# Performance work log

Measured on AMD Instinct MI355X. Metric: run time of the kernel, lower is better.

Reference implementation:

```python
import jax, jax.numpy as jnp
import numpy as np

HIDDEN = 3072
N_HEADS = 24
N_KV = 8
HEAD_DIM = HIDDEN // N_HEADS          # 128
ROT = int(HEAD_DIM * 0.75)            # 96 (partial rotary)
OP_SIZE = N_HEADS * HEAD_DIM + 2 * N_KV * HEAD_DIM  # 5120
LORA_R = 256
LORA_SCALE = 512.0 / LORA_R           # 2.0
ROPE_THETA = 10000.0
SCALE = HEAD_DIM ** -0.5


def setup_inputs() -> dict:
    key = jax.random.key(0)
    ks = jax.random.split(key, 8)
    B, S = 2, 2048
    hidden_states = jax.random.normal(ks[0], (B, S, HIDDEN), dtype=jnp.float32)
    position_ids = jnp.arange(B * S, dtype=jnp.int64 if jax.config.jax_enable_x64 else jnp.int32).reshape(B, S)
    w = lambda k, o, i: jax.random.normal(k, (o, i), dtype=jnp.float32) * (i ** -0.5)
    return {
        "hidden_states": hidden_states,
        "Wqkv": w(ks[1], OP_SIZE, HIDDEN),
        "Aqkv": w(ks[2], LORA_R, HIDDEN),
        "Bqkv": w(ks[3], OP_SIZE, LORA_R) * 0.01,
        "Wo": w(ks[4], HIDDEN, N_HEADS * HEAD_DIM),
        "Ao": w(ks[5], LORA_R, N_HEADS * HEAD_DIM),
        "Bo": w(ks[6], HIDDEN, LORA_R) * 0.01,
        "position_ids": position_ids,
    }


def _lora_linear(x, W, A, Bm):
    # base GEMM + low-rank LoRA update, scaling = alpha/r
    return x @ W.T + (x @ A.T) @ Bm.T * LORA_SCALE


def _rotate_half(x):
    h = x.shape[-1] // 2
    return jnp.concatenate((-x[..., h:], x[..., :h]), axis=-1)


def reference(hidden_states, Wqkv, Aqkv, Bqkv, Wo, Ao, Bo, position_ids):
    B, S, _ = hidden_states.shape
    qkv = _lora_linear(hidden_states, Wqkv, Aqkv, Bqkv)  # [B,S,5120]
    q_pos = N_HEADS * HEAD_DIM
    kv_pos = N_KV * HEAD_DIM
    q = qkv[..., :q_pos].reshape(B, S, N_HEADS, HEAD_DIM)
    k = qkv[..., q_pos:q_pos + kv_pos].reshape(B, S, N_KV, HEAD_DIM)
    v = qkv[..., q_pos + kv_pos:].reshape(B, S, N_KV, HEAD_DIM)

    # partial RoPE: cos/sin cache over rotary_ndims=96
    inv_freq = 1.0 / (ROPE_THETA ** (jnp.arange(0, ROT, 2, dtype=jnp.float32) / ROT))  # [48]
    freqs = position_ids.astype(jnp.float32)[..., None] * inv_freq  # [B,S,48]
    emb = jnp.concatenate((freqs, freqs), axis=-1)                   # [B,S,96]
    cos = jnp.cos(emb)[:, :, None, :]  # broadcast over head axis (bsnd)
    sin = jnp.sin(emb)[:, :, None, :]

    def rope(x):
        xr, xp = x[..., :ROT], x[..., ROT:]
        xr = xr * cos + _rotate_half(xr) * sin
        return jnp.concatenate((xr, xp), axis=-1)

    q = rope(q)
    k = rope(k)

    # GQA: repeat kv heads to match query heads
    groups = N_HEADS // N_KV
    k = jnp.repeat(k, groups, axis=2)
    v = jnp.repeat(v, groups, axis=2)

    scores = jnp.einsum('bqhd,bkhd->bhqk', q, k) * SCALE  # [B,H,S,S]
    causal = jnp.tril(jnp.ones((S, S), dtype=bool))
    scores = jnp.where(causal, scores, jnp.finfo(scores.dtype).min)
    probs = jax.nn.softmax(scores, axis=-1)
    attn = jnp.einsum('bhqk,bkhd->bqhd', probs, v).reshape(B, S, N_HEADS * HEAD_DIM)
    return _lora_linear(attn, Wo, Ao, Bo)
```

## Files before the change

kernel.cpp:

```cpp
#include <hip/hip_runtime.h>

typedef unsigned short u16;
typedef unsigned int   u32;

typedef __bf16 bf16_t;
typedef bf16_t bf16x8 __attribute__((ext_vector_type(8)));
typedef float  f32x4  __attribute__((ext_vector_type(4)));
typedef float  f32x16 __attribute__((ext_vector_type(16)));
typedef u16    u16x8  __attribute__((ext_vector_type(8)));
typedef u32    u32x4  __attribute__((ext_vector_type(4)));

__device__ __forceinline__ float bf2f(u16 u) { return __uint_as_float(((u32)u) << 16); }
__device__ __forceinline__ u16 f2bf(float f) {
  u32 u = __float_as_uint(f);
  u32 r = u + 0x7fffu + ((u >> 16) & 1u);
  return (u16)(r >> 16);
}
__device__ __forceinline__ float fast_exp2(float x) { return __builtin_amdgcn_exp2f(x); }

__device__ __forceinline__ void gload_lds16(const u16* g, u16* l) {
  __builtin_amdgcn_global_load_lds(
      (const __attribute__((address_space(1))) void*)g,
      (__attribute__((address_space(3))) void*)l,
      16, 0, 0);
}

#define SBAR0() __builtin_amdgcn_sched_barrier(0)
#define HWBAR() __builtin_amdgcn_s_barrier()

__global__ void k_cast_all(const float* __restrict__ x,  const float* __restrict__ wq,
                           const float* __restrict__ bq, const float* __restrict__ aq,
                           const float* __restrict__ wo, const float* __restrict__ bo,
                           const float* __restrict__ ao,
                           u16* __restrict__ xw, u16* __restrict__ wwq, u16* __restrict__ aqkvb,
                           u16* __restrict__ wwo, u16* __restrict__ aob) {
  const int total = 5177344;
  int i = blockIdx.x * blockDim.x + threadIdx.x;
  const int stride = gridDim.x * blockDim.x;
  for (; i < total; i += stride) {
    const float* src; u16* dst; int C8, L, off, loc;
    if      (i < 1572864) { src = x;  dst = xw;    C8 = 384; L = 3328; off = 0;    loc = i; }
    else if (i < 3538944) { src = wq; dst = wwq;   C8 = 384; L = 3328; off = 0;    loc = i - 1572864; }
    else if (i < 3702784) { src = bq; dst = wwq;   C8 = 32;  L = 3328; off = 3072; loc = i - 3538944; }
    else if (i < 3801088) { src = aq; dst = aqkvb; C8 = 384; L = 3072; off = 0;    loc = i - 3702784; }
    else if (i < 4980736) { src = wo; dst = wwo;   C8 = 384; L = 3328; off = 0;    loc = i - 3801088; }
    else if (i < 5079040) { src = bo; dst = wwo;   C8 = 32;  L = 3328; off = 3072; loc = i - 4980736; }
    else                  { src = ao; dst = aob;   C8 = 384; L = 3072; off = 0;    loc = i - 5079040; }
    const int r = loc / C8, c8 = loc - r * C8;
    const f32x4* p = (const f32x4*)(src + ((size_t)r * C8 + c8) * 8);
    f32x4 a = p[0], b2 = p[1];
    u16x8 o;
    o[0] = f2bf(a[0]);  o[1] = f2bf(a[1]);  o[2] = f2bf(a[2]);  o[3] = f2bf(a[3]);
    o[4] = f2bf(b2[0]); o[5] = f2bf(b2[1]); o[6] = f2bf(b2[2]); o[7] = f2bf(b2[3]);
    *(u16x8*)(dst + (size_t)r * L + off + c8 * 8) = o;
  }
}

__global__ void k_red4_cast(const float* __restrict__ t4, u16* __restrict__ out,
                            int C8, int L, int off, float scale, size_t plane) {
  const int r  = blockIdx.y;
  const int c8 = blockIdx.x * 64 + threadIdx.x;
  if (c8 >= C8) return;
  size_t base = (size_t)r * (C8 * 8) + c8 * 8;
  float s[8];
#pragma unroll
  for (int j = 0; j < 8; ++j) s[j] = 0.f;
#pragma unroll
  for (int p = 0; p < 4; ++p) {
    const f32x4* q = (const f32x4*)(t4 + p * plane + base);
    f32x4 a = q[0], b = q[1];
    s[0] += a[0]; s[1] += a[1]; s[2] += a[2]; s[3] += a[3];
    s[4] += b[0]; s[5] += b[1]; s[6] += b[2]; s[7] += b[3];
  }
  u16x8 o;
#pragma unroll
  for (int j = 0; j < 8; ++j) o[j] = f2bf(s[j] * scale);
  *(u16x8*)(out + (size_t)r * L + off + c8 * 8) = o;
}

__global__ __launch_bounds__(256) void k_gemm_bt_sk(
    const u16* __restrict__ A, const u16* __restrict__ B, float* __restrict__ C,
    int M, int N, int lda, int ldb, int kc) {
  __shared__ u16 As[64][64 + 8];
  __shared__ u16 Bs[64][64 + 8];
  const int tid   = threadIdx.x;
  const int lane  = tid & 63;
  const int w     = tid >> 6;
  const int wm    = (w >> 1) * 32;
  const int wn    = (w & 1) * 32;
  const int row16 = lane & 15;
  const int quad  = lane >> 4;
  const int m0 = blockIdx.y * 64;
  const int n0 = blockIdx.x * 64;
  const int ldr = tid >> 2;
  const int ldc = (tid & 3) * 16;
  const int z   = blockIdx.z;
  float* Cz = C + (size_t)z * M * N;
  const int kbeg = z * kc, kend = kbeg + kc;

  f32x4 acc[2][2] = {};

  for (int k0 = kbeg; k0 < kend; k0 += 64) {
    const u16* ga = A + (size_t)(m0 + ldr) * lda + (k0 + ldc);
    const u16* gb = B + (size_t)(n0 + ldr) * ldb + (k0 + ldc);
    u16x8 a0 = *(const u16x8*)ga;
    u16x8 a1 = *(const u16x8*)(ga + 8);
    u16x8 b0 = *(const u16x8*)gb;
    u16x8 b1 = *(const u16x8*)(gb + 8);
    __syncthreads();
    *(u16x8*)&As[ldr][ldc]     = a0;
    *(u16x8*)&As[ldr][ldc + 8] = a1;
    *(u16x8*)&Bs[ldr][ldc]     = b0;
    *(u16x8*)&Bs[ldr][ldc + 8] = b1;
    __syncthreads();
#pragma unroll
    for (int kk = 0; kk < 64; kk += 32) {
      bf16x8 af0 = *(const bf16x8*)&As[wm + row16][kk + quad * 8];
      bf16x8 af1 = *(const bf16x8*)&As[wm + 16 + row16][kk + quad * 8];
      bf16x8 bg0 = *(const bf16x8*)&Bs[wn + row16][kk + quad * 8];
      bf16x8 bg1 = *(const bf16x8*)&Bs[wn + 16 + row16][kk + quad * 8];
      acc[0][0] = __builtin_amdgcn_mfma_f32_16x16x32_bf16(af0, bg0, acc[0][0], 0, 0, 0);
      acc[0][1] = __builtin_amdgcn_mfma_f32_16x16x32_bf16(af0, bg1, acc[0][1], 0, 0, 0);
      acc[1][0] = __builtin_amdgcn_mfma_f32_16x16x32_bf16(af1, bg0, acc[1][0], 0, 0, 0);
      acc[1][1] = __builtin_amdgcn_mfma_f32_16x16x32_bf16(af1, bg1, acc[1][1], 0, 0, 0);
    }
  }
#pragma unroll
  for (int tm = 0; tm < 2; ++tm)
#pragma unroll
    for (int tn = 0; tn < 2; ++tn) {
      int gm = m0 + wm + tm * 16 + quad * 4;
      int gn = n0 + wn + tn * 16 + row16;
#pragma unroll
      for (int r = 0; r < 4; ++r)
        Cz[(size_t)(gm + r) * N + gn] = acc[tm][tn][r];
    }
}

__device__ __forceinline__ void stage_half(
    int H, int nt4,
    const u16* __restrict__ A, const u16* __restrict__ B, int K,
    int m0, int n0, u16* AsB, u16* BsB,
    int w, int rowin, int colsw) {
  if (H >= nt4) return;
  const int t = H >> 2, slot = H & 3;
  const int half = slot & 1;
  const u16* G = (slot < 2) ? A : B;
  const int r0 = (slot < 2) ? m0 : n0;
  u16* lds = ((slot < 2) ? AsB : BsB) + (t & 1) * 16384 + half * 8192;
  const int k0 = t * 64;
#pragma unroll
  for (int i = 0; i < 2; ++i) {
    const int chunk = w * 2 + i;
    const int row = half * 128 + chunk * 8 + rowin;
    gload_lds16(G + (size_t)(r0 + row) * K + k0 + colsw, lds + chunk * 512);
  }
}

__device__ __forceinline__ bf16x8 frag_ld(const u16* base, int row, int c16) {
  return *(const bf16x8*)(base + row * 64 + ((c16 ^ (row & 7)) << 3));
}

template <int RB>
__device__ __forceinline__ void gemm256_group(
    int k, int nt,
    const u16* __restrict__ A, const u16* __restrict__ B, int K,
    int m0, int n0, u16* AsB, u16* BsB,
    int wr, int wc, int row16, int quad, int w, int rowin, int colsw,
    f32x4 (&acc)[8][4]) {
  const u16* Ab = AsB + RB * 16384;
  const u16* Bb = BsB + RB * 16384;
  const int nt4 = nt * 4;
  bf16x8 a0[4][2], a1[4][2], b0[2][2], b1[2][2];

#pragma unroll
  for (int mf = 0; mf < 4; ++mf)
#pragma unroll
    for (int kk = 0; kk < 2; ++kk)
      a0[mf][kk] = frag_ld(Ab, wr * 128 + mf * 16 + row16, kk * 4 + quad);
#pragma unroll
  for (int nf = 0; nf < 2; ++nf)
#pragma unroll
    for (int kk = 0; kk < 2; ++kk)
      b0[nf][kk] = frag_ld(Bb, wc * 64 + nf * 16 + row16, kk * 4 + quad);
  stage_half(4 * k + 5, nt4, A, B, K, m0, n0, AsB, BsB, w, rowin, colsw);
  SBAR0(); HWBAR(); SBAR0();
  __builtin_amdgcn_s_setprio(1);
#pragma unroll
  for (int mf = 0; mf < 4; ++mf)
#pragma unroll
    for (int nf = 0; nf < 2; ++nf)
#pragma unroll
      for (int kk = 0; kk < 2; ++kk)
        acc[mf][nf] = __builtin_amdgcn_mfma_f32_16x16x32_bf16(a0[mf][kk], b0[nf][kk], acc[mf][nf], 0, 0, 0);
  __builtin_amdgcn_s_setprio(0);
  SBAR0(); HWBAR(); SBAR0();

#pragma unroll
  for (int nf = 0; nf < 2; ++nf)
#pragma unroll
    for (int kk = 0; kk < 2; ++kk)
      b1[nf][kk] = frag_ld(Bb, wc * 64 + 32 + nf * 16 + row16, kk * 4 + quad);
  stage_half(4 * k + 6, nt4, A, B, K, m0, n0, AsB, BsB, w, rowin, colsw);
  SBAR0(); HWBAR(); SBAR0();
  __builtin_amdgcn_s_setprio(1);
#pragma unroll
  for (int mf = 0; mf < 4; ++mf)
#pragma unroll
    for (int nf = 0; nf < 2; ++nf)
#pragma unroll
      for (int kk = 0; kk < 2; ++kk)
        acc[mf][2 + nf] = __builtin_amdgcn_mfma_f32_16x16x32_bf16(a0[mf][kk], b1[nf][kk], acc[mf][2 + nf], 0, 0, 0);
  __builtin_amdgcn_s_setprio(0);
  SBAR0(); HWBAR(); SBAR0();

#pragma unroll
  for (int mf = 0; mf < 4; ++mf)
#pragma unroll
    for (int kk = 0; kk < 2; ++kk)
      a1[mf][kk] = frag_ld(Ab, wr * 128 + 64 + mf * 16 + row16, kk * 4 + quad);
  stage_half(4 * k + 7, nt4, A, B, K, m0, n0, AsB, BsB, w, rowin, colsw);
  SBAR0(); HWBAR(); SBAR0();
  __builtin_amdgcn_s_setprio(1);
#pragma unroll
  for (int mf = 0; mf < 4; ++mf)
#pragma unroll
    for (int nf = 0; nf < 2; ++nf)
#pragma unroll
      for (int kk = 0; kk < 2; ++kk)
        acc[4 + mf][nf] = __builtin_amdgcn_mfma_f32_16x16x32_bf16(a1[mf][kk], b0[nf][kk], acc[4 + mf][nf], 0, 0, 0);
  __builtin_amdgcn_s_setprio(0);
  SBAR0(); HWBAR(); SBAR0();

  stage_half(4 * k + 8, nt4, A, B, K, m0, n0, AsB, BsB, w, rowin, colsw);
  SBAR0();
  if (k < nt - 2) { asm volatile("s_waitcnt vmcnt(2)" ::: "memory"); }
  else            { asm volatile("s_waitcnt vmcnt(0)" ::: "memory"); }
  HWBAR(); SBAR0();
  __builtin_amdgcn_s_setprio(1);
#pragma unroll
  for (int mf = 0; mf < 4; ++mf)
#pragma unroll
    for (int nf = 0; nf < 2; ++nf)
#pragma unroll
      for (int kk = 0; kk < 2; ++kk)
        acc[4 + mf][2 + nf] = __builtin_amdgcn_mfma_f32_16x16x32_bf16(a1[mf][kk], b1[nf][kk], acc[4 + mf][2 + nf], 0, 0, 0);
  __builtin_amdgcn_s_setprio(0);
  SBAR0(); HWBAR(); SBAR0();
}

__global__ __launch_bounds__(512, 2) void k_gemm256(
    const u16* __restrict__ A, const u16* __restrict__ B, float* __restrict__ C,
    int M, int N, int K) {
  __shared__ u16 As[2 * 16384];
  __shared__ u16 Bs[2 * 16384];

  const int tid   = threadIdx.x;
  const int lane  = tid & 63;
  const int w     = tid >> 6;
  const int wr    = w >> 2;
  const int wc    = w & 3;
  const int row16 = lane & 15;
  const int quad  = lane >> 4;
  const int rowin = lane >> 3;
  const int colsw = ((lane & 7) ^ (lane >> 3)) << 3;

  const int nwg = (int)gridDim.x;
  const int bid = (int)blockIdx.x;
  const int xcd = bid & 7, rest = bid >> 3;
  const int qq = nwg >> 3, rr = nwg & 7;
  const int wg = (xcd < rr ? xcd * (qq + 1) : rr * (qq + 1) + (xcd - rr) * qq) + rest;
  const int nbx = N >> 8;
  const int m0 = (wg / nbx) << 8;
  const int n0 = (wg % nbx) << 8;

  const int nt = K >> 6;
  f32x4 acc[8][4] = {};

#pragma unroll
  for (int H = 0; H < 5; ++H)
    stage_half(H, nt * 4, A, B, K, m0, n0, As, Bs, w, rowin, colsw);
  asm volatile("s_waitcnt vmcnt(2)" ::: "memory");
  HWBAR(); SBAR0();

  int k = 0;
  for (; k + 1 < nt; k += 2) {
    gemm256_group<0>(k,     nt, A, B, K, m0, n0, As, Bs, wr, wc, row16, quad, w, rowin, colsw, acc);
    gemm256_group<1>(k + 1, nt, A, B, K, m0, n0, As, Bs, wr, wc, row16, quad, w, rowin, colsw, acc);
  }
  if (k < nt)
    gemm256_group<0>(k, nt, A, B, K, m0, n0, As, Bs, wr, wc, row16, quad, w, rowin, colsw, acc);

#pragma unroll
  for (int mi = 0; mi < 8; ++mi) {
    const int gm = m0 + wr * 128 + mi * 16 + quad * 4;
#pragma unroll
    for (int nj = 0; nj < 4; ++nj) {
      const int gn = n0 + wc * 64 + nj * 16 + row16;
#pragma unroll
      for (int r = 0; r < 4; ++r)
        C[(size_t)(gm + r) * N + gn] = acc[mi][nj][r];
    }
  }
}

__global__ void k_rope_tab(const int* __restrict__ pos_ids, float* __restrict__ tab) {
  const int t = threadIdx.x;
  const int r = blockIdx.x * 4 + t / 48;
  const int j = t % 48;
  const float pos = (float)pos_ids[r];
  float invf = powf(10000.0f, -(float)j * (1.0f / 48.0f));
  float e = pos * invf;
  tab[(size_t)r * 96 + j]      = cosf(e);
  tab[(size_t)r * 96 + 48 + j] = sinf(e);
}

__global__ void k_rope_v(const float* __restrict__ qkv, const float* __restrict__ tab,
                         u16* __restrict__ qb, u16* __restrict__ kb, u16* __restrict__ vtg) {
  const int y = blockIdx.y;
  const int d = threadIdx.x;
  if (y < 32) {
    const int r  = blockIdx.x;
    const int hh = y;
    const float* src;
    if (hh < 24) src = qkv + (size_t)r * 5120 + hh * 128;
    else         src = qkv + (size_t)r * 5120 + 3072 + (hh - 24) * 128;
    float x = src[d];
    float outv;
    if (d >= 96) {
      outv = x;
    } else {
      int j = (d < 48) ? d : d - 48;
      float c  = tab[(size_t)r * 96 + j];
      float sn = tab[(size_t)r * 96 + 48 + j];
      if (d < 48) outv = x * c - src[d + 48] * sn;
      else        outv = x * c + src[d - 48] * sn;
    }
    u16 o = f2bf(outv);
    if (hh < 24) qb[((size_t)r * 24 + hh) * 128 + d] = o;
    else         kb[((size_t)r * 8 + (hh - 24)) * 128 + d] = o;
  } else {
    const int bk = blockIdx.x >> 8;
    const int kg = blockIdx.x & 255;
    const int b = bk >> 3, kvh = bk & 7;
    const float* src = qkv + (size_t)(b * 2048 + kg * 8) * 5120 + 4096 + kvh * 128 + d;
    u16x8 pack;
#pragma unroll
    for (int t = 0; t < 8; ++t) pack[t] = f2bf(src[(size_t)t * 5120]);
    *(u16x8*)(vtg + ((size_t)bk * 128 + d) * 2048 + kg * 8) = pack;
  }
}

__global__ __launch_bounds__(256, 4) void k_attn_mfma(
    const u16* __restrict__ qb, const u16* __restrict__ kb, const u16* __restrict__ vtg,
    u16* __restrict__ attnw) {
  __shared__ u16 Ks[8192];
  __shared__ u16 Vt[2][8192];

  const int tid  = threadIdx.x;
  const int lane = tid & 63;
  const int w    = tid >> 6;
  const int l31  = lane & 31;
  const int hi   = lane >> 5;
  const int r7   = lane & 7;
  const int qt   = (int)gridDim.x - 1 - (int)blockIdx.x;
  const int bh   = blockIdx.y;
  const int b    = bh / 24;
  const int h    = bh % 24;
  const int kvh  = h / 3;
  const int q0   = qt * 128;
  const int qrow = q0 + w * 32 + l31;

  const u16* qrb    = qb + (((size_t)(b * 2048 + qrow)) * 24 + h) * 128;
  const u16* kbbase = kb + ((size_t)(b * 2048) * 8 + kvh) * 128;
  const u16* vtbase = vtg + (size_t)(b * 8 + kvh) * 128 * 2048;

  f32x16 o32[4] = {};
  float m_st = -INFINITY, l_st = 0.f;
  const float C1 = 0.08838834764831845f * 1.4426950408889634f;
  const int ntile = 2 * qt + 2;

#define STAGE_K(KB0)                                                            \
  { _Pragma("unroll") for (int i = 0; i < 4; ++i) {                             \
      const int c = w * 4 + i;                                                  \
      const int rowk = 4 * c + (lane >> 4);                                     \
      gload_lds16(kbbase + (size_t)((KB0) + rowk) * 1024 +                      \
                      (((lane & 15) ^ (rowk & 7)) << 3),                        \
                  Ks + c * 512); } }
#define STAGE_V(Vd, KB0)                                                        \
  { _Pragma("unroll") for (int i = 0; i < 4; ++i) {                             \
      const int c = w * 4 + i;                                                  \
      const int rowv = 8 * c + (lane >> 3);                                     \
      gload_lds16(vtbase + (size_t)rowv * 2048 + (KB0) +                        \
                      (((lane & 7) ^ (rowv & 7)) << 3),                         \
                  (Vd) + c * 512); } }

  STAGE_K(0);
  STAGE_V(Vt[0], 0);
  asm volatile("s_waitcnt vmcnt(0)" ::: "memory");
  SBAR0(); HWBAR(); SBAR0();

  for (int t = 0; t < ntile; ++t) {
    const int kb0 = t * 64;
    const u16* Vc = Vt[t & 1];
    if (t + 1 < ntile) STAGE_V(Vt[(t + 1) & 1], kb0 + 64);
    SBAR0();

    f32x16 s0 = {}, s1 = {};
    {
      bf16x8 qa[4];
#pragma unroll
      for (int kk = 0; kk < 4; ++kk) qa[kk] = *(const bf16x8*)(qrb + kk * 16 + hi * 8);
      __builtin_amdgcn_s_setprio(1);
#pragma unroll
      for (int kk = 0; kk < 4; ++kk) {
        bf16x8 kf0 = *(const bf16x8*)&Ks[l31 * 128 + (((2 * kk + hi) ^ r7) << 3)];
        s0 = __builtin_amdgcn_mfma_f32_32x32x16_bf16(kf0, qa[kk], s0, 0, 0, 0);
        bf16x8 kf1 = *(const bf16x8*)&Ks[(32 + l31) * 128 + (((2 * kk + hi) ^ ((32 + l31) & 7)) << 3)];
        s1 = __builtin_amdgcn_mfma_f32_32x32x16_bf16(kf1, qa[kk], s1, 0, 0, 0);
      }
      __builtin_amdgcn_s_setprio(0);
#pragma unroll
      for (int kk = 0; kk < 4; ++kk) qa[kk] = *(const bf16x8*)(qrb + 64 + kk * 16 + hi * 8);
      __builtin_amdgcn_s_setprio(1);
#pragma unroll
      for (int kk = 4; kk < 8; ++kk) {
        bf16x8 kf0 = *(const bf16x8*)&Ks[l31 * 128 + (((2 * kk + hi) ^ r7) << 3)];
        s0 = __builtin_amdgcn_mfma_f32_32x32x16_bf16(kf0, qa[kk - 4], s0, 0, 0, 0);
        bf16x8 kf1 = *(const bf16x8*)&Ks[(32 + l31) * 128 + (((2 * kk + hi) ^ ((32 + l31) & 7)) << 3)];
        s1 = __builtin_amdgcn_mfma_f32_32x32x16_bf16(kf1, qa[kk - 4], s1, 0, 0, 0);
      }
      __builtin_amdgcn_s_setprio(0);
    }

    SBAR0(); HWBAR(); SBAR0();
    if (t + 1 < ntile) STAGE_K(kb0 + 64);
    SBAR0();

    if (kb0 >= q0) {
#pragma unroll
      for (int r = 0; r < 16; ++r) {
        const int crow = (r & 3) + 8 * (r >> 2) + 4 * hi;
        if (kb0 + crow > qrow)      s0[r] = -INFINITY;
        if (kb0 + 32 + crow > qrow) s1[r] = -INFINITY;
      }
    }

    float tm[8];
#pragma unroll
    for (int r = 0; r < 8; ++r)
      tm[r] = fmaxf(fmaxf(s0[r], s0[r + 8]), fmaxf(s1[r], s1[r + 8]));
#pragma unroll
    for (int st = 4; st >= 1; st >>= 1)
#pragma unroll
      for (int r = 0; r < 4; ++r)
        if (r < st) tm[r] = fmaxf(tm[r], tm[r + st]);
    float mx = fmaxf(tm[0], __shfl_xor(tm[0], 32));

    const bool skip = __all((mx - m_st) * C1 <= 8.0f);
    if (!skip) {
      const float mnew = fmaxf(m_st, mx);
      const float alpha = fast_exp2((m_st - mnew) * C1);
      l_st *= alpha;
#pragma unroll
      for (int dt = 0; dt < 4; ++dt)
#pragma unroll
        for (int r = 0; r < 16; ++r) o32[dt][r] *= alpha;
      m_st = mnew;
    }
    const float mc = m_st * C1;
    float ts[8];
#pragma unroll
    for (int r = 0; r < 16; ++r) {
      s0[r] = fast_exp2(__builtin_fmaf(s0[r], C1, -mc));
      s1[r] = fast_exp2(__builtin_fmaf(s1[r], C1, -mc));
    }
#pragma unroll
    for (int r = 0; r < 8; ++r) ts[r] = (s0[r] + s0[r + 8]) + (s1[r] + s1[r + 8]);
#pragma unroll
    for (int st = 4; st >= 1; st >>= 1)
#pragma unroll
      for (int r = 0; r < 4; ++r)
        if (r < st) ts[r] += ts[r + st];
    l_st += ts[0] + __shfl_xor(ts[0], 32);

#pragma unroll
    for (int kt = 0; kt < 2; ++kt) {
      const f32x16& sv = kt ? s1 : s0;
      u32 pk[8];
#pragma unroll
      for (int i = 0; i < 8; ++i)
        asm("v_cvt_pk_bf16_f32 %0, %1, %2"
            : "=v"(pk[i]) : "v"(sv[2 * i]), "v"(sv[2 * i + 1]));
      u32 e0 = __shfl_xor(hi ? pk[0] : pk[2], 32);
      u32 e1 = __shfl_xor(hi ? pk[1] : pk[3], 32);
      u32 e2 = __shfl_xor(hi ? pk[4] : pk[6], 32);
      u32 e3 = __shfl_xor(hi ? pk[5] : pk[7], 32);
      u32x4 w0, w1;
      w0[0] = hi ? e0 : pk[0]; w0[1] = hi ? e1 : pk[1];
      w0[2] = hi ? pk[2] : e0; w0[3] = hi ? pk[3] : e1;
      w1[0] = hi ? e2 : pk[4]; w1[1] = hi ? e3 : pk[5];
      w1[2] = hi ? pk[6] : e2; w1[3] = hi ? pk[7] : e3;
      bf16x8 pb0 = __builtin_bit_cast(bf16x8, w0);
      bf16x8 pb1 = __builtin_bit_cast(bf16x8, w1);
      __builtin_amdgcn_s_setprio(1);
#pragma unroll
      for (int dt = 0; dt < 4; ++dt) {
        const int vrow = dt * 32 + l31;
        bf16x8 vf0 = *(const bf16x8*)&Vc[vrow * 64 + (((2 * (2 * kt) + hi) ^ (vrow & 7)) << 3)];
        o32[dt] = __builtin_amdgcn_mfma_f32_32x32x16_bf16(vf0, pb0, o32[dt], 0, 0, 0);
        bf16x8 vf1 = *(const bf16x8*)&Vc[vrow * 64 + (((2 * (2 * kt + 1) + hi) ^ (vrow & 7)) << 3)];
        o32[dt] = __builtin_amdgcn_mfma_f32_32x32x16_bf16(vf1, pb1, o32[dt], 0, 0, 0);
      }
      __builtin_amdgcn_s_setprio(0);
    }

    asm volatile("s_waitcnt vmcnt(0)" ::: "memory");
    SBAR0(); HWBAR(); SBAR0();
  }

  const float inv = 1.0f / l_st;
  u16* scr = Vt[w >> 1] + (w & 1) * 4096;
#pragma unroll
  for (int dt = 0; dt < 4; ++dt)
#pragma unroll
    for (int r = 0; r < 16; ++r) {
      const int d = 32 * dt + (r & 3) + 8 * (r >> 2) + 4 * hi;
      const int slot = (d >> 3) ^ (l31 & 7);
      scr[l31 * 128 + slot * 8 + (d & 7)] = f2bf(o32[dt][r] * inv);
    }
  const int q32r = lane >> 1, part = lane & 1;
  const size_t grow = ((size_t)(b * 2048 + q0 + w * 32 + q32r)) * 3328 + (size_t)h * 128;
#pragma unroll
  for (int c = 0; c < 8; ++c) {
    const int d0 = part * 64 + c * 8;
    const int s2 = (d0 >> 3) ^ (q32r & 7);
    *(u16x8*)(attnw + grow + d0) = *(const u16x8*)&scr[q32r * 128 + s2 * 8];
  }
}

#define OFF_XW    ((size_t)0)
#define OFF_WWQ   ((size_t)27262976)
#define OFF_AQKVB ((size_t)61341696)
#define OFF_WWO   ((size_t)62914560)
#define OFF_AOB   ((size_t)83361792)
#define OFF_QKV   ((size_t)84934656)
#define OFF_TA4   OFF_QKV
#define OFF_QB    OFF_XW
#define OFF_KB    OFF_WWQ
#define OFF_VTG   (OFF_WWQ + (size_t)8388608)
#define OFF_RTAB  (OFF_WWQ + (size_t)16777216)
#define OFF_ATTNW OFF_QKV
#define OFF_TO4   (OFF_QKV + (size_t)27262976)

extern "C" void kernel_launch(void* const* d_in, const int* in_sizes, int n_in,
                              void* d_out, int out_size, void* d_ws, size_t ws_size,
                              hipStream_t stream) {
  const float* x    = (const float*)d_in[0];
  const float* Wqkv = (const float*)d_in[1];
  const float* Aqkv = (const float*)d_in[2];
  const float* Bqkv = (const float*)d_in[3];
  const float* Wo   = (const float*)d_in[4];
  const float* Ao   = (const float*)d_in[5];
  const float* Bo   = (const float*)d_in[6];
  const int*   pos  = (const int*)d_in[7];
  float* out = (float*)d_out;
  char* ws = (char*)d_ws;

  u16* xw    = (u16*)(ws + OFF_XW);
  u16* wwq   = (u16*)(ws + OFF_WWQ);
  u16* aqkvb = (u16*)(ws + OFF_AQKVB);
  u16* wwo   = (u16*)(ws + OFF_WWO);
  u16* aob   = (u16*)(ws + OFF_AOB);
  float* qkv = (float*)(ws + OFF_QKV);
  float* tA4 = (float*)(ws + OFF_TA4);
  u16* qb    = (u16*)(ws + OFF_QB);
  u16* kb    = (u16*)(ws + OFF_KB);
  u16* vtg   = (u16*)(ws + OFF_VTG);
  float* rtab = (float*)(ws + OFF_RTAB);
  u16* attnw = (u16*)(ws + OFF_ATTNW);
  float* tO4 = (float*)(ws + OFF_TO4);

  k_cast_all<<<2048, 256, 0, stream>>>(x, Wqkv, Bqkv, Aqkv, Wo, Bo, Ao,
                                       xw, wwq, aqkvb, wwo, aob);

  k_gemm_bt_sk<<<dim3(4, 64, 4), 256, 0, stream>>>(xw, aqkvb, tA4, 4096, 256, 3328, 3072, 768);
  k_red4_cast<<<dim3(1, 4096), 64, 0, stream>>>(tA4, xw, 32, 3328, 3072, 2.f, (size_t)4096 * 256);

  k_gemm256<<<dim3((5120 / 256) * (4096 / 256)), 512, 0, stream>>>(xw, wwq, qkv, 4096, 5120, 3328);

  k_rope_tab<<<dim3(1024), 192, 0, stream>>>(pos, rtab);
  k_rope_v<<<dim3(4096, 33), 128, 0, stream>>>(qkv, rtab, qb, kb, vtg);

  k_attn_mfma<<<dim3(16, 48), 256, 0, stream>>>(qb, kb, vtg, attnw);

  k_gemm_bt_sk<<<dim3(4, 64, 4), 256, 0, stream>>>(attnw, aob, tO4, 4096, 256, 3328, 3072, 768);
  k_red4_cast<<<dim3(1, 4096), 64, 0, stream>>>(tO4, attnw, 32, 3328, 3072, 2.f, (size_t)4096 * 256);

  k_gemm256<<<dim3((3072 / 256) * (4096 / 256)), 512, 0, stream>>>(attnw, wwo, out, 4096, 3072, 3328);
}
```

Baseline: 744.4 us.

## Double-buffer K and V tiles with one barrier per iteration in attention

The attention kernel now double-buffers both K and V in LDS, prefetching the next K and V tiles together after a single wait and barrier at the top of each iteration, instead of single-buffered K with a mid-iteration barrier. Q fragments are loaded once into registers before the loop rather than reloaded every tile. The launch-bounds occupancy hint is dropped and LDS grows to 64KB, which may lower occupancy while raising register pressure. The cast kernel also simplifies its source indexing, using shifts for the narrow LoRA-B blocks.

After: 740.4 us. Within noise of the previous version (-0.5%).

```diff
diff --git a/kernel.cpp b/kernel.cpp
--- a/kernel.cpp
+++ b/kernel.cpp
@@ -38,16 +38,15 @@
   int i = blockIdx.x * blockDim.x + threadIdx.x;
   const int stride = gridDim.x * blockDim.x;
   for (; i < total; i += stride) {
-    const float* src; u16* dst; int C8, L, off, loc;
-    if      (i < 1572864) { src = x;  dst = xw;    C8 = 384; L = 3328; off = 0;    loc = i; }
-    else if (i < 3538944) { src = wq; dst = wwq;   C8 = 384; L = 3328; off = 0;    loc = i - 1572864; }
-    else if (i < 3702784) { src = bq; dst = wwq;   C8 = 32;  L = 3328; off = 3072; loc = i - 3538944; }
-    else if (i < 3801088) { src = aq; dst = aqkvb; C8 = 384; L = 3072; off = 0;    loc = i - 3702784; }
-    else if (i < 4980736) { src = wo; dst = wwo;   C8 = 384; L = 3328; off = 0;    loc = i - 3801088; }
-    else if (i < 5079040) { src = bo; dst = wwo;   C8 = 32;  L = 3328; off = 3072; loc = i - 4980736; }
-    else                  { src = ao; dst = aob;   C8 = 384; L = 3072; off = 0;    loc = i - 5079040; }
-    const int r = loc / C8, c8 = loc - r * C8;
-    const f32x4* p = (const f32x4*)(src + ((size_t)r * C8 + c8) * 8);
+    const float* src; u16* dst; int r, c8, L, off, sL;
+    if (i < 1572864)      { int loc = i;           r = loc / 384; c8 = loc - r * 384; src = x;  dst = xw;    L = 3328; off = 0;    sL = 3072; }
+    else if (i < 3538944) { int loc = i - 1572864; r = loc / 384; c8 = loc - r * 384; src = wq; dst = wwq;   L = 3328; off = 0;    sL = 3072; }
+    else if (i < 3702784) { int loc = i - 3538944; r = loc >> 5;  c8 = loc & 31;      src = bq; dst = wwq;   L = 3328; off = 3072; sL = 256;  }
+    else if (i < 3801088) { int loc = i - 3702784; r = loc / 384; c8 = loc - r * 384; src = aq; dst = aqkvb; L = 3072; off = 0;    sL = 3072; }
+    else if (i < 4980736) { int loc = i - 3801088; r = loc / 384; c8 = loc - r * 384; src = wo; dst = wwo;   L = 3328; off = 0;    sL = 3072; }
+    else if (i < 5079040) { int loc = i - 4980736; r = loc >> 5;  c8 = loc & 31;      src = bo; dst = wwo;   L = 3328; off = 3072; sL = 256;  }
+    else                  { int loc = i - 5079040; r = loc / 384; c8 = loc - r * 384; src = ao; dst = aob;   L = 3072; off = 0;    sL = 3072; }
+    const f32x4* p = (const f32x4*)(src + (size_t)r * sL + c8 * 8);
     f32x4 a = p[0], b2 = p[1];
     u16x8 o;
     o[0] = f2bf(a[0]);  o[1] = f2bf(a[1]);  o[2] = f2bf(a[2]);  o[3] = f2bf(a[3]);
@@ -351,11 +350,11 @@
   }
 }
 
-__global__ __launch_bounds__(256, 4) void k_attn_mfma(
+__global__ __launch_bounds__(256) void k_attn_mfma(
     const u16* __restrict__ qb, const u16* __restrict__ kb, const u16* __restrict__ vtg,
     u16* __restrict__ attnw) {
-  __shared__ u16 Ks[8192];
-  __shared__ u16 Vt[2][8192];
+  __shared__ u16 Ks0[8192], Ks1[8192];
+  __shared__ u16 Vt0[8192], Vt1[8192];
 
   const int tid  = threadIdx.x;
   const int lane = tid & 63;
@@ -371,7 +370,11 @@
   const int q0   = qt * 128;
   const int qrow = q0 + w * 32 + l31;
 
-  const u16* qrb    = qb + (((size_t)(b * 2048 + qrow)) * 24 + h) * 128;
+  const u16* qrb = qb + (((size_t)(b * 2048 + qrow)) * 24 + h) * 128;
+  bf16x8 qf[8];
+#pragma unroll
+  for (int kk = 0; kk < 8; ++kk) qf[kk] = *(const bf16x8*)(qrb + kk * 16 + hi * 8);
+
   const u16* kbbase = kb + ((size_t)(b * 2048) * 8 + kvh) * 128;
   const u16* vtbase = vtg + (size_t)(b * 8 + kvh) * 128 * 2048;
 
@@ -380,13 +383,13 @@
   const float C1 = 0.08838834764831845f * 1.4426950408889634f;
   const int ntile = 2 * qt + 2;
 
-#define STAGE_K(KB0)                                                            \
+#define STAGE_K(Kd, KB0)                                                        \
   { _Pragma("unroll") for (int i = 0; i < 4; ++i) {                             \
       const int c = w * 4 + i;                                                  \
       const int rowk = 4 * c + (lane >> 4);                                     \
       gload_lds16(kbbase + (size_t)((KB0) + rowk) * 1024 +                      \
                       (((lane & 15) ^ (rowk & 7)) << 3),                        \
-                  Ks + c * 512); } }
+                  (Kd) + c * 512); } }
 #define STAGE_V(Vd, KB0)                                                        \
   { _Pragma("unroll") for (int i = 0; i < 4; ++i) {                             \
       const int c = w * 4 + i;                                                  \
@@ -395,47 +398,34 @@
                       (((lane & 7) ^ (rowv & 7)) << 3),                         \
                   (Vd) + c * 512); } }
 
-  STAGE_K(0);
-  STAGE_V(Vt[0], 0);
-  asm volatile("s_waitcnt vmcnt(0)" ::: "memory");
-  SBAR0(); HWBAR(); SBAR0();
+  STAGE_K(Ks0, 0);
+  STAGE_V(Vt0, 0);
 
   for (int t = 0; t < ntile; ++t) {
     const int kb0 = t * 64;
-    const u16* Vc = Vt[t & 1];
-    if (t + 1 < ntile) STAGE_V(Vt[(t + 1) & 1], kb0 + 64);
+    const u16* Kc = (t & 1) ? Ks1 : Ks0;
+    const u16* Vc = (t & 1) ? Vt1 : Vt0;
+
+    asm volatile("s_waitcnt vmcnt(0)" ::: "memory");
+    SBAR0(); HWBAR(); SBAR0();
+    if (t + 1 < ntile) {
+      u16* Kn = (t & 1) ? Ks0 : Ks1;
+      u16* Vn = (t & 1) ? Vt0 : Vt1;
+      STAGE_K(Kn, kb0 + 64);
+      STAGE_V(Vn, kb0 + 64);
+    }
     SBAR0();
 
     f32x16 s0 = {}, s1 = {};
-    {
-      bf16x8 qa[4];
-#pragma unroll
-      for (int kk = 0; kk < 4; ++kk) qa[kk] = *(const bf16x8*)(qrb + kk * 16 + hi * 8);
-      __builtin_amdgcn_s_setprio(1);
-#pragma unroll
-      for (int kk = 0; kk < 4; ++kk) {
-        bf16x8 kf0 = *(const bf16x8*)&Ks[l31 * 128 + (((2 * kk + hi) ^ r7) << 3)];
-        s0 = __builtin_amdgcn_mfma_f32_32x32x16_bf16(kf0, qa[kk], s0, 0, 0, 0);
-        bf16x8 kf1 = *(const bf16x8*)&Ks[(32 + l31) * 128 + (((2 * kk + hi) ^ ((32 + l31) & 7)) << 3)];
-        s1 = __builtin_amdgcn_mfma_f32_32x32x16_bf16(kf1, qa[kk], s1, 0, 0, 0);
-      }
-      __builtin_amdgcn_s_setprio(0);
-#pragma unroll
-      for (int kk = 0; kk < 4; ++kk) qa[kk] = *(const bf16x8*)(qrb + 64 + kk * 16 + hi * 8);
-      __builtin_amdgcn_s_setprio(1);
-#pragma unroll
-      for (int kk = 4; kk < 8; ++kk) {
-        bf16x8 kf0 = *(const bf16x8*)&Ks[l31 * 128 + (((2 * kk + hi) ^ r7) << 3)];
-        s0 = __builtin_amdgcn_mfma_f32_32x32x16_bf16(kf0, qa[kk - 4], s0, 0, 0, 0);
-        bf16x8 kf1 = *(const bf16x8*)&Ks[(32 + l31) * 128 + (((2 * kk + hi) ^ ((32 + l31) & 7)) << 3)];
-        s1 = __builtin_amdgcn_mfma_f32_32x32x16_bf16(kf1, qa[kk - 4], s1, 0, 0, 0);
-      }
-      __builtin_amdgcn_s_setprio(0);
-    }
-
-    SBAR0(); HWBAR(); SBAR0();
-    if (t + 1 < ntile) STAGE_K(kb0 + 64);
-    SBAR0();
+    __builtin_amdgcn_s_setprio(1);
+#pragma unroll
+    for (int kk = 0; kk < 8; ++kk) {
+      bf16x8 kf0 = *(const bf16x8*)&Kc[l31 * 128 + (((2 * kk + hi) ^ r7) << 3)];
+      s0 = __builtin_amdgcn_mfma_f32_32x32x16_bf16(kf0, qf[kk], s0, 0, 0, 0);
+      bf16x8 kf1 = *(const bf16x8*)&Kc[(32 + l31) * 128 + (((2 * kk + hi) ^ ((32 + l31) & 7)) << 3)];
+      s1 = __builtin_amdgcn_mfma_f32_32x32x16_bf16(kf1, qf[kk], s1, 0, 0, 0);
+    }
+    __builtin_amdgcn_s_setprio(0);
 
     if (kb0 >= q0) {
 #pragma unroll
@@ -514,13 +504,11 @@
       }
       __builtin_amdgcn_s_setprio(0);
     }
-
-    asm volatile("s_waitcnt vmcnt(0)" ::: "memory");
-    SBAR0(); HWBAR(); SBAR0();
-  }
-
+  }
+
+  __syncthreads();
   const float inv = 1.0f / l_st;
-  u16* scr = Vt[w >> 1] + (w & 1) * 4096;
+  u16* scr = ((w < 2) ? Ks0 : Ks1) + (w & 1) * 4096;
 #pragma unroll
   for (int dt = 0; dt < 4; ++dt)
 #pragma unroll
```
